# Performance work log

Hardware: AMD Instinct MI355X
Metric: run time of the kernel (lower is better)

## Reference

```python
import jax, jax.numpy as jnp
import numpy as np

NEG_SLOPE = 0.2  # LeakyReLU slope used by GAT attention
EPS = 1e-16


def gat_conv(x, edge_index, W, a_src, a_dst, b):
    """One GATConv layer with 'mean' head aggregation.
    x: [N, Fin], edge_index: [2, E] (row 0 = src/j, row 1 = dst/i),
    W: [Fin, H*F], a_src/a_dst: [H, F], b: [F].
    Returns [N, F].
    """
    N = x.shape[0]
    H, F = a_src.shape
    h = (x @ W).reshape(N, H, F)                      # [N, H, F]
    src, dst = edge_index[0], edge_index[1]
    # per-node attention halves, gathered per edge
    as_ = jnp.einsum('nhf,hf->nh', h, a_src)          # [N, H]
    ad_ = jnp.einsum('nhf,hf->nh', h, a_dst)          # [N, H]
    e = jax.nn.leaky_relu(as_[src] + ad_[dst], NEG_SLOPE)  # [E, H]
    # segment softmax over incoming edges of each dst node
    m = jax.ops.segment_max(e, dst, num_segments=N)   # [N, H]
    ex = jnp.exp(e - m[dst])                          # [E, H]
    denom = jax.ops.segment_sum(ex, dst, num_segments=N)
    alpha = ex / (denom[dst] + EPS)                   # [E, H]
    # weighted scatter-aggregate of source features
    out = jax.ops.segment_sum(alpha[:, :, None] * h[src], dst, num_segments=N)  # [N, H, F]
    return out.mean(axis=1) + b                       # mean over heads


def setup_inputs() -> dict:
    key = jax.random.key(0)
    ks = jax.random.split(key, 10)
    N, E = 100000, 1000000
    in_dim, hid, out_dim, H = 128, 32, 16, 4
    x = jax.random.normal(ks[0], (N, in_dim), dtype=jnp.float32)
    edge_index = jax.random.randint(ks[1], (2, E), 0, N, dtype=jnp.int64)
    s1 = 1.0 / np.sqrt(in_dim)
    s2 = 1.0 / np.sqrt(hid)
    W1 = jax.random.uniform(ks[2], (in_dim, H * hid), jnp.float32, -s1, s1)
    a1_src = jax.random.uniform(ks[3], (H, hid), jnp.float32, -s2, s2)
    a1_dst = jax.random.uniform(ks[4], (H, hid), jnp.float32, -s2, s2)
    b1 = jnp.zeros((hid,), jnp.float32)
    s3 = 1.0 / np.sqrt(out_dim)
    W2 = jax.random.uniform(ks[5], (hid, H * out_dim), jnp.float32, -s2, s2)
    a2_src = jax.random.uniform(ks[6], (H, out_dim), jnp.float32, -s3, s3)
    a2_dst = jax.random.uniform(ks[7], (H, out_dim), jnp.float32, -s3, s3)
    b2 = jnp.zeros((out_dim,), jnp.float32)
    return {"x": x, "edge_index": edge_index,
            "W1": W1, "a1_src": a1_src, "a1_dst": a1_dst, "b1": b1,
            "W2": W2, "a2_src": a2_src, "a2_dst": a2_dst, "b2": b2}


def reference(x, edge_index, W1, a1_src, a1_dst, b1, W2, a2_src, a2_dst, b2):
    h = gat_conv(x, edge_index, W1, a1_src, a1_dst, b1)
    h = jax.nn.relu(h)
    # dropout is identity in eval mode
    out = gat_conv(h, edge_index, W2, a2_src, a2_dst, b2)
    return out
```

## Files before the change

### kernel.cpp

```cpp
#include <hip/hip_runtime.h>
#include <math.h>

#define NEG_SLOPE 0.2f
#define EPS_GAT 1e-16f
#define LOG2E 1.4426950408889634f
typedef unsigned int u32;
typedef unsigned short u16;
typedef __attribute__((ext_vector_type(8))) short short8;
typedef __attribute__((ext_vector_type(4))) float f32x4;

__device__ inline u16 f2bf(float x) {
    union { float f; u32 u; } v; v.f = x;
    u32 r = v.u + 0x7FFFu + ((v.u >> 16) & 1u);
    return (u16)(r >> 16);
}
__device__ inline float bf_lo(u32 u) {
    union { u32 i; float f; } v; v.i = u << 16; return v.f;
}
__device__ inline float bf_hi(u32 u) {
    union { u32 i; float f; } v; v.i = u & 0xFFFF0000u; return v.f;
}
__device__ inline float bf1(u16 s) {
    union { u32 i; float f; } v; v.i = ((u32)s) << 16; return v.f;
}
__device__ inline float fast_exp2(float x) {
#if __has_builtin(__builtin_amdgcn_exp2f)
    return __builtin_amdgcn_exp2f(x);
#else
    return exp2f(x);
#endif
}
__device__ inline float lrelu_exp2(float t) {
    return fast_exp2(fmaxf(t, NEG_SLOPE * t));
}


__global__ void degree_kernel(const int* __restrict__ dst, int E,
                              int* __restrict__ counts, int* __restrict__ rank) {
    int e = blockIdx.x * blockDim.x + threadIdx.x;
    if (e < E) rank[e] = atomicAdd(&counts[dst[e]], 1);
}

__global__ __launch_bounds__(1024) void scan_block_kernel(const int* __restrict__ counts, int N,
                                                          int* __restrict__ scanned, int* __restrict__ bsums) {
    __shared__ int tmp[1024];
    int i = blockIdx.x * 1024 + threadIdx.x;
    int v = (i < N) ? counts[i] : 0;
    tmp[threadIdx.x] = v;
    __syncthreads();
    for (int d = 1; d < 1024; d <<= 1) {
        int t = (threadIdx.x >= d) ? tmp[threadIdx.x - d] : 0;
        __syncthreads();
        tmp[threadIdx.x] += t;
        __syncthreads();
    }
    if (i < N) scanned[i] = tmp[threadIdx.x];
    if (threadIdx.x == 1023) bsums[blockIdx.x] = tmp[1023];
}

__global__ __launch_bounds__(256) void scan_partials_kernel(int* __restrict__ bsums, int nb) {
    __shared__ int tmp[256];
    int tid = threadIdx.x;
    int v = (tid < nb) ? bsums[tid] : 0;
    tmp[tid] = v;
    __syncthreads();
    for (int d = 1; d < 256; d <<= 1) {
        int t = (tid >= d) ? tmp[tid - d] : 0;
        __syncthreads();
        tmp[tid] += t;
        __syncthreads();
    }
    if (tid < nb) bsums[tid] = tmp[tid] - v;
}

__global__ void finalize_offsets_kernel(const int* __restrict__ scanned,
                                        const int* __restrict__ bsums_excl, int N,
                                        int* __restrict__ row_off) {
    int i = blockIdx.x * blockDim.x + threadIdx.x;
    if (i < N) {
        int incl = scanned[i] + bsums_excl[i >> 10];
        row_off[i + 1] = incl;
        if (i == 0) row_off[0] = 0;
    }
}

__global__ void fill_csr_kernel(const int* __restrict__ src, const int* __restrict__ dst, int E,
                                const int* __restrict__ row_off, const int* __restrict__ rank,
                                int* __restrict__ csr_src) {
    int e = blockIdx.x * blockDim.x + threadIdx.x;
    if (e < E) {
        int pos = row_off[dst[e]] + rank[e];
        csr_src[pos] = src[e];
    }
}


__global__ void prep_kernel(const float* __restrict__ W1,
                            u16* __restrict__ w1t_hi, u16* __restrict__ w1t_lo,
                            const float* __restrict__ W2, const float* __restrict__ a2s,
                            const float* __restrict__ a2d, float* __restrict__ w_as,
                            float* __restrict__ w_ad) {
    if (blockIdx.x < 64) {
        int i = blockIdx.x * 256 + threadIdx.x;
        int k = i >> 7, n = i & 127;
        float w = W1[i];
        u16 hi = f2bf(w);
        u16 lo = f2bf(w - bf1(hi));
        w1t_hi[n * 128 + k] = hi;
        w1t_lo[n * 128 + k] = lo;
    } else {
        int t = threadIdx.x;
        if (t < 128) {
            int h = t >> 5, k = t & 31;
            float s1 = 0.f, s2 = 0.f;
#pragma unroll
            for (int f = 0; f < 16; ++f) {
                float w = W2[k * 64 + h * 16 + f];
                s1 += w * a2s[h * 16 + f];
                s2 += w * a2d[h * 16 + f];
            }
            w_as[h * 32 + k] = s1;
            w_ad[h * 32 + k] = s2;
        }
    }
}


__global__ __launch_bounds__(256) void gemm1_mfma_kernel(const float* __restrict__ X,
                                                         const u16* __restrict__ w1t_hi,
                                                         const u16* __restrict__ w1t_lo,
                                                         u16* __restrict__ Hb, int N) {
    __shared__ u16 xsh_hi[64][40];
    __shared__ u16 xsh_lo[64][40];
    __shared__ u16 wsh_hi[128][40];
    __shared__ u16 wsh_lo[128][40];
    int tid = threadIdx.x;
    int wave = tid >> 6, lane = tid & 63, quad = lane >> 4;
    int m0 = blockIdx.x * 64;

    f32x4 acc[4][2];
#pragma unroll
    for (int rt = 0; rt < 4; ++rt)
#pragma unroll
        for (int ct = 0; ct < 2; ++ct) acc[rt][ct] = (f32x4)(0.f);

    int xrow = tid >> 2, xkq = (tid & 3) * 8;

    for (int k0 = 0; k0 < 128; k0 += 32) {
        {
            int gr = m0 + xrow;
            float f[8];
            *(float4*)&f[0] = (gr < N) ? *(const float4*)(X + (size_t)gr * 128 + k0 + xkq)
                                       : make_float4(0.f, 0.f, 0.f, 0.f);
            *(float4*)&f[4] = (gr < N) ? *(const float4*)(X + (size_t)gr * 128 + k0 + xkq + 4)
                                       : make_float4(0.f, 0.f, 0.f, 0.f);
            u16 hi[8], lo[8];
#pragma unroll
            for (int i = 0; i < 8; ++i) {
                hi[i] = f2bf(f[i]);
                lo[i] = f2bf(f[i] - bf1(hi[i]));
            }
            *(uint4*)&xsh_hi[xrow][xkq] = *(uint4*)hi;
            *(uint4*)&xsh_lo[xrow][xkq] = *(uint4*)lo;
        }
        {
#pragma unroll
            for (int i = 0; i < 2; ++i) {
                int id = tid * 2 + i;
                int n = id >> 2, part = id & 3;
                *(uint4*)&wsh_hi[n][part * 8] =
                    ((const uint4*)(w1t_hi + n * 128 + k0))[part];
                *(uint4*)&wsh_lo[n][part * 8] =
                    ((const uint4*)(w1t_lo + n * 128 + k0))[part];
            }
        }
        __syncthreads();

        short8 bhi[2], blo[2];
#pragma unroll
        for (int ct = 0; ct < 2; ++ct) {
            int n = wave * 32 + ct * 16 + (lane & 15);
            bhi[ct] = *(const short8*)&wsh_hi[n][quad * 8];
            blo[ct] = *(const short8*)&wsh_lo[n][quad * 8];
        }
#pragma unroll
        for (int rt = 0; rt < 4; ++rt) {
            int m = rt * 16 + (lane & 15);
            short8 ahi = *(const short8*)&xsh_hi[m][quad * 8];
            short8 alo = *(const short8*)&xsh_lo[m][quad * 8];
#pragma unroll
            for (int ct = 0; ct < 2; ++ct) {
                acc[rt][ct] = __builtin_amdgcn_mfma_f32_16x16x32_bf16(ahi, bhi[ct], acc[rt][ct], 0, 0, 0);
                acc[rt][ct] = __builtin_amdgcn_mfma_f32_16x16x32_bf16(alo, bhi[ct], acc[rt][ct], 0, 0, 0);
                acc[rt][ct] = __builtin_amdgcn_mfma_f32_16x16x32_bf16(ahi, blo[ct], acc[rt][ct], 0, 0, 0);
            }
        }
        __syncthreads();
    }

#pragma unroll
    for (int rt = 0; rt < 4; ++rt)
#pragma unroll
        for (int ct = 0; ct < 2; ++ct) {
            int col = wave * 32 + ct * 16 + (lane & 15);
#pragma unroll
            for (int r = 0; r < 4; ++r) {
                int gr = m0 + rt * 16 + quad * 4 + r;
                if (gr < N) Hb[(size_t)gr * 128 + col] = f2bf(acc[rt][ct][r]);
            }
        }
}


__global__ void attn1_kernel(const u16* __restrict__ Hb, const float* __restrict__ a_src,
                             const float* __restrict__ a_dst, float* __restrict__ as_,
                             float* __restrict__ ad_, int N) {
    int t = blockIdx.x * blockDim.x + threadIdx.x;
    int n = t >> 2, h = t & 3;
    if (n >= N) return;
    const u32* hr = (const u32*)(Hb + (size_t)n * 128 + h * 32);
    const float* av = a_src + h * 32;
    const float* bv = a_dst + h * 32;
    float s1 = 0.f, s2 = 0.f;
#pragma unroll
    for (int q = 0; q < 4; ++q) {
        uint4 u = *(const uint4*)(hr + q * 4);
        float f0 = bf_lo(u.x), f1 = bf_hi(u.x);
        float f2 = bf_lo(u.y), f3 = bf_hi(u.y);
        float f4 = bf_lo(u.z), f5 = bf_hi(u.z);
        float f6 = bf_lo(u.w), f7 = bf_hi(u.w);
        int k = q * 8;
        s1 += f0 * av[k] + f1 * av[k + 1] + f2 * av[k + 2] + f3 * av[k + 3]
            + f4 * av[k + 4] + f5 * av[k + 5] + f6 * av[k + 6] + f7 * av[k + 7];
        s2 += f0 * bv[k] + f1 * bv[k + 1] + f2 * bv[k + 2] + f3 * bv[k + 3]
            + f4 * bv[k + 4] + f5 * bv[k + 5] + f6 * bv[k + 6] + f7 * bv[k + 7];
    }
    as_[n * 4 + h] = s1 * LOG2E;
    ad_[n * 4 + h] = s2 * LOG2E;
}


__global__ __launch_bounds__(256) void node_agg128_kernel(const u32* __restrict__ Hb,
                                                          const float* __restrict__ as_,
                                                          const float* __restrict__ ad_,
                                                          const int* __restrict__ row_off,
                                                          const int* __restrict__ csr_src,
                                                          const float* __restrict__ bias,
                                                          u32* __restrict__ O1, int N) {
    int lane = threadIdx.x & 63;
    int node = __builtin_amdgcn_readfirstlane(blockIdx.x * 4 + (threadIdx.x >> 6));
    if (node >= N) return;
    int start = __builtin_amdgcn_readfirstlane(row_off[node]);
    int end   = __builtin_amdgcn_readfirstlane(row_off[node + 1]);
    int deg = end - start;
    int h = lane >> 4;
    float adh = ad_[node * 4 + h];

    int clamp = (deg > 0) ? deg - 1 : 0;
    int vidx = csr_src[start + min(lane, clamp)];
    int m = min(deg, 64);

    float ax = 0.f, ay = 0.f, den = 0.f;
    int j = 0;
    for (; j + 4 <= m; j += 4) {
        int s0 = __builtin_amdgcn_readlane(vidx, j);
        int s1 = __builtin_amdgcn_readlane(vidx, j + 1);
        int s2 = __builtin_amdgcn_readlane(vidx, j + 2);
        int s3 = __builtin_amdgcn_readlane(vidx, j + 3);
        float a0 = as_[s0 * 4 + h], a1 = as_[s1 * 4 + h];
        float a2 = as_[s2 * 4 + h], a3 = as_[s3 * 4 + h];
        u32 u0 = Hb[s0 * 64 + lane];
        u32 u1 = Hb[s1 * 64 + lane];
        u32 u2 = Hb[s2 * 64 + lane];
        u32 u3 = Hb[s3 * 64 + lane];
        float e0 = lrelu_exp2(a0 + adh), e1 = lrelu_exp2(a1 + adh);
        float e2 = lrelu_exp2(a2 + adh), e3 = lrelu_exp2(a3 + adh);
        ax += e0 * bf_lo(u0); ay += e0 * bf_hi(u0); den += e0;
        ax += e1 * bf_lo(u1); ay += e1 * bf_hi(u1); den += e1;
        ax += e2 * bf_lo(u2); ay += e2 * bf_hi(u2); den += e2;
        ax += e3 * bf_lo(u3); ay += e3 * bf_hi(u3); den += e3;
    }
    for (; j < m; ++j) {
        int s = __builtin_amdgcn_readlane(vidx, j);
        float e = lrelu_exp2(as_[s * 4 + h] + adh);
        u32 u = Hb[s * 64 + lane];
        ax += e * bf_lo(u); ay += e * bf_hi(u); den += e;
    }
    for (int jj = start + 64; jj < end; ++jj) {
        int s = __builtin_amdgcn_readfirstlane(csr_src[jj]);
        float e = lrelu_exp2(as_[s * 4 + h] + adh);
        u32 u = Hb[s * 64 + lane];
        ax += e * bf_lo(u); ay += e * bf_hi(u); den += e;
    }
    float inv = 1.f / (den + EPS_GAT);
    float px = ax * inv, py = ay * inv;
    px += __shfl_xor(px, 16); py += __shfl_xor(py, 16);
    px += __shfl_xor(px, 32); py += __shfl_xor(py, 32);
    if (lane < 16) {
        int f = lane * 2;
        float ox = fmaxf(px * 0.25f + bias[f], 0.f);
        float oy = fmaxf(py * 0.25f + bias[f + 1], 0.f);
        O1[node * 16 + lane] = (u32)f2bf(ox) | ((u32)f2bf(oy) << 16);
    }
}


__global__ void attn2_kernel(const u32* __restrict__ O1, const float* __restrict__ w_as,
                             const float* __restrict__ w_ad, float* __restrict__ as_,
                             float* __restrict__ ad_, int N) {
    int t = blockIdx.x * blockDim.x + threadIdx.x;
    int n = t >> 2, h = t & 3;
    if (n >= N) return;
    const u32* r = O1 + (size_t)n * 16;
    const float* wa = w_as + h * 32;
    const float* wd = w_ad + h * 32;
    float s1 = 0.f, s2 = 0.f;
#pragma unroll
    for (int q = 0; q < 4; ++q) {
        uint4 u = *(const uint4*)(r + q * 4);
        float f0 = bf_lo(u.x), f1 = bf_hi(u.x);
        float f2 = bf_lo(u.y), f3 = bf_hi(u.y);
        float f4 = bf_lo(u.z), f5 = bf_hi(u.z);
        float f6 = bf_lo(u.w), f7 = bf_hi(u.w);
        int k = q * 8;
        s1 += f0 * wa[k] + f1 * wa[k + 1] + f2 * wa[k + 2] + f3 * wa[k + 3]
            + f4 * wa[k + 4] + f5 * wa[k + 5] + f6 * wa[k + 6] + f7 * wa[k + 7];
        s2 += f0 * wd[k] + f1 * wd[k + 1] + f2 * wd[k + 2] + f3 * wd[k + 3]
            + f4 * wd[k + 4] + f5 * wd[k + 5] + f6 * wd[k + 6] + f7 * wd[k + 7];
    }
    as_[n * 4 + h] = s1 * LOG2E;
    ad_[n * 4 + h] = s2 * LOG2E;
}


__global__ __launch_bounds__(256) void node_agg32_fused_kernel(const u32* __restrict__ O1,
                                                               const float* __restrict__ as_,
                                                               const float* __restrict__ ad_,
                                                               const int* __restrict__ row_off,
                                                               const int* __restrict__ csr_src,
                                                               const float* __restrict__ W2,
                                                               const float* __restrict__ b2,
                                                               float* __restrict__ Out, int N) {
    __shared__ float w2sh[2048];
    __shared__ float aggsh[4][136];
    int tid = threadIdx.x;
    {
        float4 v = ((const float4*)W2)[tid];
        *(float4*)&w2sh[tid * 4] = v;
        float4 v2 = ((const float4*)W2)[tid + 256];
        *(float4*)&w2sh[(tid + 256) * 4] = v2;
    }

    int lane = tid & 63;
    int nb = tid >> 6;
    int node = __builtin_amdgcn_readfirstlane(blockIdx.x * 4 + nb);
    bool active = node < N;
    int h = lane >> 4, f = lane & 15;
    if (active) {
        int start = __builtin_amdgcn_readfirstlane(row_off[node]);
        int end   = __builtin_amdgcn_readfirstlane(row_off[node + 1]);
        int deg = end - start;
        float adh = ad_[node * 4 + h];

        int clamp = (deg > 0) ? deg - 1 : 0;
        int vidx = csr_src[start + min(lane, clamp)];
        int m = min(deg, 64);

        float ax = 0.f, ay = 0.f, den = 0.f;
        int j = 0;
        for (; j + 4 <= m; j += 4) {
            int s0 = __builtin_amdgcn_readlane(vidx, j);
            int s1 = __builtin_amdgcn_readlane(vidx, j + 1);
            int s2 = __builtin_amdgcn_readlane(vidx, j + 2);
            int s3 = __builtin_amdgcn_readlane(vidx, j + 3);
            float a0 = as_[s0 * 4 + h], a1 = as_[s1 * 4 + h];
            float a2 = as_[s2 * 4 + h], a3 = as_[s3 * 4 + h];
            u32 u0 = O1[s0 * 16 + f];
            u32 u1 = O1[s1 * 16 + f];
            u32 u2 = O1[s2 * 16 + f];
            u32 u3 = O1[s3 * 16 + f];
            float e0 = lrelu_exp2(a0 + adh), e1 = lrelu_exp2(a1 + adh);
            float e2 = lrelu_exp2(a2 + adh), e3 = lrelu_exp2(a3 + adh);
            ax += e0 * bf_lo(u0); ay += e0 * bf_hi(u0); den += e0;
            ax += e1 * bf_lo(u1); ay += e1 * bf_hi(u1); den += e1;
            ax += e2 * bf_lo(u2); ay += e2 * bf_hi(u2); den += e2;
            ax += e3 * bf_lo(u3); ay += e3 * bf_hi(u3); den += e3;
        }
        for (; j < m; ++j) {
            int s = __builtin_amdgcn_readlane(vidx, j);
            float e = lrelu_exp2(as_[s * 4 + h] + adh);
            u32 u = O1[s * 16 + f];
            ax += e * bf_lo(u); ay += e * bf_hi(u); den += e;
        }
        for (int jj = start + 64; jj < end; ++jj) {
            int s = __builtin_amdgcn_readfirstlane(csr_src[jj]);
            float e = lrelu_exp2(as_[s * 4 + h] + adh);
            u32 u = O1[s * 16 + f];
            ax += e * bf_lo(u); ay += e * bf_hi(u); den += e;
        }
        float inv = 1.f / (den + EPS_GAT);
        aggsh[nb][h * 34 + f * 2]     = ax * inv;
        aggsh[nb][h * 34 + f * 2 + 1] = ay * inv;
    }
    __syncthreads();

    if (active) {
        int q = h, o = f;
        float s = 0.f;
#pragma unroll
        for (int k = 0; k < 32; ++k)
            s += aggsh[nb][q * 34 + k] * w2sh[k * 64 + q * 16 + o];
        s += __shfl_xor(s, 16);
        s += __shfl_xor(s, 32);
        if (lane < 16)
            Out[(size_t)node * 16 + o] = s * 0.25f + b2[o];
    }
}


extern "C" void kernel_launch(void* const* d_in, const int* in_sizes, int n_in,
                              void* d_out, int out_size, void* d_ws, size_t ws_size,
                              hipStream_t stream) {
    const float* x      = (const float*)d_in[0];
    const int*   eidx   = (const int*)d_in[1];
    const float* W1     = (const float*)d_in[2];
    const float* a1_src = (const float*)d_in[3];
    const float* a1_dst = (const float*)d_in[4];
    const float* b1     = (const float*)d_in[5];
    const float* W2     = (const float*)d_in[6];
    const float* a2_src = (const float*)d_in[7];
    const float* a2_dst = (const float*)d_in[8];
    const float* b2     = (const float*)d_in[9];
    float* out = (float*)d_out;

    const int N = in_sizes[0] / 128;
    const int E = in_sizes[1] / 2;
    const int* src = eidx;
    const int* dst = eidx + E;

    char* base = (char*)d_ws;
    size_t off = 0;
    auto carve = [&](size_t bytes) -> char* {
        off = (off + 255) & ~(size_t)255;
        char* p = base + off;
        off += bytes;
        return p;
    };
    int* counts   = (int*)carve((size_t)N * 4);
    int* scanned  = (int*)carve((size_t)N * 4);
    int* bsums    = (int*)carve(256 * 4);
    int* row_off  = (int*)carve((size_t)(N + 1) * 4);
    int* rank     = (int*)carve((size_t)E * 4);
    int* csr_src  = (int*)carve((size_t)E * 4);
    u16* w1t_hi   = (u16*)carve(128 * 128 * 2);
    u16* w1t_lo   = (u16*)carve(128 * 128 * 2);
    u16* h1b      = (u16*)carve((size_t)N * 128 * 2);
    u32* out1b    = (u32*)carve((size_t)N * 16 * 4);
    float* as1  = (float*)carve((size_t)N * 4 * 4);
    float* ad1  = (float*)carve((size_t)N * 4 * 4);
    float* as2  = (float*)carve((size_t)N * 4 * 4);
    float* ad2  = (float*)carve((size_t)N * 4 * 4);
    float* w_as = (float*)carve(4 * 32 * 4);
    float* w_ad = (float*)carve(4 * 32 * 4);
    (void)ws_size; (void)n_in; (void)out_size;

    hipMemsetAsync(counts, 0, (size_t)N * 4, stream);
    degree_kernel<<<(E + 255) / 256, 256, 0, stream>>>(dst, E, counts, rank);
    int nb = (N + 1023) / 1024;
    scan_block_kernel<<<nb, 1024, 0, stream>>>(counts, N, scanned, bsums);
    scan_partials_kernel<<<1, 256, 0, stream>>>(bsums, nb);
    finalize_offsets_kernel<<<(N + 255) / 256, 256, 0, stream>>>(scanned, bsums, N, row_off);
    fill_csr_kernel<<<(E + 255) / 256, 256, 0, stream>>>(src, dst, E, row_off, rank, csr_src);

    prep_kernel<<<65, 256, 0, stream>>>(W1, w1t_hi, w1t_lo, W2, a2_src, a2_dst, w_as, w_ad);

    gemm1_mfma_kernel<<<(N + 63) / 64, 256, 0, stream>>>(x, w1t_hi, w1t_lo, h1b, N);
    attn1_kernel<<<(N * 4 + 255) / 256, 256, 0, stream>>>(h1b, a1_src, a1_dst, as1, ad1, N);
    node_agg128_kernel<<<(N + 3) / 4, 256, 0, stream>>>((const u32*)h1b, as1, ad1,
                                                        row_off, csr_src, b1, out1b, N);

    attn2_kernel<<<(N * 4 + 255) / 256, 256, 0, stream>>>(out1b, w_as, w_ad, as2, ad2, N);
    node_agg32_fused_kernel<<<(N + 3) / 4, 256, 0, stream>>>(out1b, as2, ad2, row_off,
                                                             csr_src, W2, b2, out, N);
}
```

Baseline: 322.9 us.

## Fuse attention-score kernels into GEMM and layer-1 aggregation, merge prep with degree

```diff
diff --git a/kernel.cpp b/kernel.cpp
--- a/kernel.cpp
+++ b/kernel.cpp
@@ -35,73 +35,19 @@
 }
 
 
-__global__ void degree_kernel(const int* __restrict__ dst, int E,
-                              int* __restrict__ counts, int* __restrict__ rank) {
-    int e = blockIdx.x * blockDim.x + threadIdx.x;
-    if (e < E) rank[e] = atomicAdd(&counts[dst[e]], 1);
-}
-
-__global__ __launch_bounds__(1024) void scan_block_kernel(const int* __restrict__ counts, int N,
-                                                          int* __restrict__ scanned, int* __restrict__ bsums) {
-    __shared__ int tmp[1024];
-    int i = blockIdx.x * 1024 + threadIdx.x;
-    int v = (i < N) ? counts[i] : 0;
-    tmp[threadIdx.x] = v;
-    __syncthreads();
-    for (int d = 1; d < 1024; d <<= 1) {
-        int t = (threadIdx.x >= d) ? tmp[threadIdx.x - d] : 0;
-        __syncthreads();
-        tmp[threadIdx.x] += t;
-        __syncthreads();
-    }
-    if (i < N) scanned[i] = tmp[threadIdx.x];
-    if (threadIdx.x == 1023) bsums[blockIdx.x] = tmp[1023];
-}
-
-__global__ __launch_bounds__(256) void scan_partials_kernel(int* __restrict__ bsums, int nb) {
-    __shared__ int tmp[256];
-    int tid = threadIdx.x;
-    int v = (tid < nb) ? bsums[tid] : 0;
-    tmp[tid] = v;
-    __syncthreads();
-    for (int d = 1; d < 256; d <<= 1) {
-        int t = (tid >= d) ? tmp[tid - d] : 0;
-        __syncthreads();
-        tmp[tid] += t;
-        __syncthreads();
-    }
-    if (tid < nb) bsums[tid] = tmp[tid] - v;
-}
-
-__global__ void finalize_offsets_kernel(const int* __restrict__ scanned,
-                                        const int* __restrict__ bsums_excl, int N,
-                                        int* __restrict__ row_off) {
-    int i = blockIdx.x * blockDim.x + threadIdx.x;
-    if (i < N) {
-        int incl = scanned[i] + bsums_excl[i >> 10];
-        row_off[i + 1] = incl;
-        if (i == 0) row_off[0] = 0;
-    }
-}
-
-__global__ void fill_csr_kernel(const int* __restrict__ src, const int* __restrict__ dst, int E,
-                                const int* __restrict__ row_off, const int* __restrict__ rank,
-                                int* __restrict__ csr_src) {
-    int e = blockIdx.x * blockDim.x + threadIdx.x;
-    if (e < E) {
-        int pos = row_off[dst[e]] + rank[e];
-        csr_src[pos] = src[e];
-    }
-}
-
-
-__global__ void prep_kernel(const float* __restrict__ W1,
-                            u16* __restrict__ w1t_hi, u16* __restrict__ w1t_lo,
-                            const float* __restrict__ W2, const float* __restrict__ a2s,
-                            const float* __restrict__ a2d, float* __restrict__ w_as,
-                            float* __restrict__ w_ad) {
-    if (blockIdx.x < 64) {
-        int i = blockIdx.x * 256 + threadIdx.x;
+__global__ void degree_prep_kernel(const int* __restrict__ dst, int E,
+                                   int* __restrict__ counts, int* __restrict__ rank,
+                                   const float* __restrict__ W1,
+                                   u16* __restrict__ w1t_hi, u16* __restrict__ w1t_lo,
+                                   const float* __restrict__ W2, const float* __restrict__ a2s,
+                                   const float* __restrict__ a2d, float* __restrict__ w_as,
+                                   float* __restrict__ w_ad, int degBlocks) {
+    int b = blockIdx.x;
+    if (b < degBlocks) {
+        int e = b * 256 + threadIdx.x;
+        if (e < E) rank[e] = atomicAdd(&counts[dst[e]], 1);
+    } else if (b < degBlocks + 64) {
+        int i = (b - degBlocks) * 256 + threadIdx.x;
         int k = i >> 7, n = i & 127;
         float w = W1[i];
         u16 hi = f2bf(w);
@@ -125,18 +71,79 @@
     }
 }
 
+__global__ __launch_bounds__(1024) void scan_block_kernel(const int* __restrict__ counts, int N,
+                                                          int* __restrict__ scanned, int* __restrict__ bsums) {
+    __shared__ int tmp[1024];
+    int i = blockIdx.x * 1024 + threadIdx.x;
+    int v = (i < N) ? counts[i] : 0;
+    tmp[threadIdx.x] = v;
+    __syncthreads();
+    for (int d = 1; d < 1024; d <<= 1) {
+        int t = (threadIdx.x >= d) ? tmp[threadIdx.x - d] : 0;
+        __syncthreads();
+        tmp[threadIdx.x] += t;
+        __syncthreads();
+    }
+    if (i < N) scanned[i] = tmp[threadIdx.x];
+    if (threadIdx.x == 1023) bsums[blockIdx.x] = tmp[1023];
+}
+
+__global__ __launch_bounds__(256) void scan_partials_kernel(int* __restrict__ bsums, int nb) {
+    __shared__ int tmp[256];
+    int tid = threadIdx.x;
+    int v = (tid < nb) ? bsums[tid] : 0;
+    tmp[tid] = v;
+    __syncthreads();
+    for (int d = 1; d < 256; d <<= 1) {
+        int t = (tid >= d) ? tmp[tid - d] : 0;
+        __syncthreads();
+        tmp[tid] += t;
+        __syncthreads();
+    }
+    if (tid < nb) bsums[tid] = tmp[tid] - v;
+}
+
+__global__ void finalize_offsets_kernel(const int* __restrict__ scanned,
+                                        const int* __restrict__ bsums_excl, int N,
+                                        int* __restrict__ row_off) {
+    int i = blockIdx.x * blockDim.x + threadIdx.x;
+    if (i < N) {
+        int incl = scanned[i] + bsums_excl[i >> 10];
+        row_off[i + 1] = incl;
+        if (i == 0) row_off[0] = 0;
+    }
+}
+
+__global__ void fill_csr_kernel(const int* __restrict__ src, const int* __restrict__ dst, int E,
+                                const int* __restrict__ row_off, const int* __restrict__ rank,
+                                int* __restrict__ csr_src) {
+    int e = blockIdx.x * blockDim.x + threadIdx.x;
+    if (e < E) {
+        int pos = row_off[dst[e]] + rank[e];
+        csr_src[pos] = src[e];
+    }
+}
+
 
 __global__ __launch_bounds__(256) void gemm1_mfma_kernel(const float* __restrict__ X,
                                                          const u16* __restrict__ w1t_hi,
                                                          const u16* __restrict__ w1t_lo,
-                                                         u16* __restrict__ Hb, int N) {
+                                                         const float* __restrict__ a_src,
+                                                         const float* __restrict__ a_dst,
+                                                         u16* __restrict__ Hb,
+                                                         float* __restrict__ as_,
+                                                         float* __restrict__ ad_, int N) {
     __shared__ u16 xsh_hi[64][40];
     __shared__ u16 xsh_lo[64][40];
-    __shared__ u16 wsh_hi[128][40];
-    __shared__ u16 wsh_lo[128][40];
+    __shared__ u16 wbuf[10240];
+    __shared__ float ash[128], adsh[128];
+    u16* wsh_hi = wbuf;
+    u16* wsh_lo = wbuf + 5120;
     int tid = threadIdx.x;
     int wave = tid >> 6, lane = tid & 63, quad = lane >> 4;
     int m0 = blockIdx.x * 64;
+
+    if (tid < 128) { ash[tid] = a_src[tid]; adsh[tid] = a_dst[tid]; }
 
     f32x4 acc[4][2];
 #pragma unroll
@@ -168,9 +175,9 @@
             for (int i = 0; i < 2; ++i) {
                 int id = tid * 2 + i;
                 int n = id >> 2, part = id & 3;
-                *(uint4*)&wsh_hi[n][part * 8] =
+                *(uint4*)&wsh_hi[n * 40 + part * 8] =
                     ((const uint4*)(w1t_hi + n * 128 + k0))[part];
-                *(uint4*)&wsh_lo[n][part * 8] =
+                *(uint4*)&wsh_lo[n * 40 + part * 8] =
                     ((const uint4*)(w1t_lo + n * 128 + k0))[part];
             }
         }
@@ -180,8 +187,8 @@
 #pragma unroll
         for (int ct = 0; ct < 2; ++ct) {
             int n = wave * 32 + ct * 16 + (lane & 15);
-            bhi[ct] = *(const short8*)&wsh_hi[n][quad * 8];
-            blo[ct] = *(const short8*)&wsh_lo[n][quad * 8];
+            bhi[ct] = *(const short8*)&wsh_hi[n * 40 + quad * 8];
+            blo[ct] = *(const short8*)&wsh_lo[n * 40 + quad * 8];
         }
 #pragma unroll
         for (int rt = 0; rt < 4; ++rt) {
@@ -198,6 +205,7 @@
         __syncthreads();
     }
 
+    const int HS = 130;
 #pragma unroll
     for (int rt = 0; rt < 4; ++rt)
 #pragma unroll
@@ -205,38 +213,32 @@
             int col = wave * 32 + ct * 16 + (lane & 15);
 #pragma unroll
             for (int r = 0; r < 4; ++r) {
-                int gr = m0 + rt * 16 + quad * 4 + r;
-                if (gr < N) Hb[(size_t)gr * 128 + col] = f2bf(acc[rt][ct][r]);
-            }
-        }
-}
-
-
-__global__ void attn1_kernel(const u16* __restrict__ Hb, const float* __restrict__ a_src,
-                             const float* __restrict__ a_dst, float* __restrict__ as_,
-                             float* __restrict__ ad_, int N) {
-    int t = blockIdx.x * blockDim.x + threadIdx.x;
-    int n = t >> 2, h = t & 3;
-    if (n >= N) return;
-    const u32* hr = (const u32*)(Hb + (size_t)n * 128 + h * 32);
-    const float* av = a_src + h * 32;
-    const float* bv = a_dst + h * 32;
-    float s1 = 0.f, s2 = 0.f;
-#pragma unroll
-    for (int q = 0; q < 4; ++q) {
-        uint4 u = *(const uint4*)(hr + q * 4);
-        float f0 = bf_lo(u.x), f1 = bf_hi(u.x);
-        float f2 = bf_lo(u.y), f3 = bf_hi(u.y);
-        float f4 = bf_lo(u.z), f5 = bf_hi(u.z);
-        float f6 = bf_lo(u.w), f7 = bf_hi(u.w);
-        int k = q * 8;
-        s1 += f0 * av[k] + f1 * av[k + 1] + f2 * av[k + 2] + f3 * av[k + 3]
-            + f4 * av[k + 4] + f5 * av[k + 5] + f6 * av[k + 6] + f7 * av[k + 7];
-        s2 += f0 * bv[k] + f1 * bv[k + 1] + f2 * bv[k + 2] + f3 * bv[k + 3]
-            + f4 * bv[k + 4] + f5 * bv[k + 5] + f6 * bv[k + 6] + f7 * bv[k + 7];
-    }
-    as_[n * 4 + h] = s1 * LOG2E;
-    ad_[n * 4 + h] = s2 * LOG2E;
+                int row = rt * 16 + quad * 4 + r;
+                u16 hv = f2bf(acc[rt][ct][r]);
+                int gr = m0 + row;
+                if (gr < N) Hb[(size_t)gr * 128 + col] = hv;
+                wbuf[row * HS + col] = hv;
+            }
+        }
+    __syncthreads();
+
+    {
+        int row = tid >> 2, h = tid & 3;
+        int gr = m0 + row;
+        if (gr < N) {
+            const u32* hr = (const u32*)&wbuf[row * HS + h * 32];
+            float s1 = 0.f, s2 = 0.f;
+#pragma unroll
+            for (int q = 0; q < 16; ++q) {
+                u32 u = hr[q];
+                float flo = bf_lo(u), fhi = bf_hi(u);
+                s1 += flo * ash[h * 32 + 2 * q] + fhi * ash[h * 32 + 2 * q + 1];
+                s2 += flo * adsh[h * 32 + 2 * q] + fhi * adsh[h * 32 + 2 * q + 1];
+            }
+            as_[(size_t)gr * 4 + h] = s1 * LOG2E;
+            ad_[(size_t)gr * 4 + h] = s2 * LOG2E;
+        }
+    }
 }
 
 
@@ -246,7 +248,11 @@
                                                           const int* __restrict__ row_off,
                                                           const int* __restrict__ csr_src,
                                                           const float* __restrict__ bias,
-                                                          u32* __restrict__ O1, int N) {
+                                                          const float* __restrict__ w_as,
+                                                          const float* __restrict__ w_ad,
+                                                          u32* __restrict__ O1,
+                                                          float* __restrict__ as2,
+                                                          float* __restrict__ ad2, int N) {
     int lane = threadIdx.x & 63;
     int node = __builtin_amdgcn_readfirstlane(blockIdx.x * 4 + (threadIdx.x >> 6));
     if (node >= N) return;
@@ -260,7 +266,8 @@
     int vidx = csr_src[start + min(lane, clamp)];
     int m = min(deg, 64);
 
-    float ax = 0.f, ay = 0.f, den = 0.f;
+    float2 acc = make_float2(0.f, 0.f);
+    float den = 0.f;
     int j = 0;
     for (; j + 4 <= m; j += 4) {
         int s0 = __builtin_amdgcn_readlane(vidx, j);
@@ -275,61 +282,48 @@
         u32 u3 = Hb[s3 * 64 + lane];
         float e0 = lrelu_exp2(a0 + adh), e1 = lrelu_exp2(a1 + adh);
         float e2 = lrelu_exp2(a2 + adh), e3 = lrelu_exp2(a3 + adh);
-        ax += e0 * bf_lo(u0); ay += e0 * bf_hi(u0); den += e0;
-        ax += e1 * bf_lo(u1); ay += e1 * bf_hi(u1); den += e1;
-        ax += e2 * bf_lo(u2); ay += e2 * bf_hi(u2); den += e2;
-        ax += e3 * bf_lo(u3); ay += e3 * bf_hi(u3); den += e3;
+        acc.x = fmaf(e0, bf_lo(u0), acc.x); acc.y = fmaf(e0, bf_hi(u0), acc.y); den += e0;
+        acc.x = fmaf(e1, bf_lo(u1), acc.x); acc.y = fmaf(e1, bf_hi(u1), acc.y); den += e1;
+        acc.x = fmaf(e2, bf_lo(u2), acc.x); acc.y = fmaf(e2, bf_hi(u2), acc.y); den += e2;
+        acc.x = fmaf(e3, bf_lo(u3), acc.x); acc.y = fmaf(e3, bf_hi(u3), acc.y); den += e3;
     }
     for (; j < m; ++j) {
         int s = __builtin_amdgcn_readlane(vidx, j);
         float e = lrelu_exp2(as_[s * 4 + h] + adh);
         u32 u = Hb[s * 64 + lane];
-        ax += e * bf_lo(u); ay += e * bf_hi(u); den += e;
+        acc.x = fmaf(e, bf_lo(u), acc.x); acc.y = fmaf(e, bf_hi(u), acc.y); den += e;
     }
     for (int jj = start + 64; jj < end; ++jj) {
         int s = __builtin_amdgcn_readfirstlane(csr_src[jj]);
         float e = lrelu_exp2(as_[s * 4 + h] + adh);
         u32 u = Hb[s * 64 + lane];
-        ax += e * bf_lo(u); ay += e * bf_hi(u); den += e;
+        acc.x = fmaf(e, bf_lo(u), acc.x); acc.y = fmaf(e, bf_hi(u), acc.y); den += e;
     }
     float inv = 1.f / (den + EPS_GAT);
-    float px = ax * inv, py = ay * inv;
+    float px = acc.x * inv, py = acc.y * inv;
     px += __shfl_xor(px, 16); py += __shfl_xor(py, 16);
     px += __shfl_xor(px, 32); py += __shfl_xor(py, 32);
-    if (lane < 16) {
-        int f = lane * 2;
-        float ox = fmaxf(px * 0.25f + bias[f], 0.f);
-        float oy = fmaxf(py * 0.25f + bias[f + 1], 0.f);
+
+    int f2 = (lane & 15) * 2;
+    float2 bv = *(const float2*)&bias[f2];
+    float ox = fmaxf(px * 0.25f + bv.x, 0.f);
+    float oy = fmaxf(py * 0.25f + bv.y, 0.f);
+    if (lane < 16)
         O1[node * 16 + lane] = (u32)f2bf(ox) | ((u32)f2bf(oy) << 16);
-    }
-}
-
-
-__global__ void attn2_kernel(const u32* __restrict__ O1, const float* __restrict__ w_as,
-                             const float* __restrict__ w_ad, float* __restrict__ as_,
-                             float* __restrict__ ad_, int N) {
-    int t = blockIdx.x * blockDim.x + threadIdx.x;
-    int n = t >> 2, h = t & 3;
-    if (n >= N) return;
-    const u32* r = O1 + (size_t)n * 16;
-    const float* wa = w_as + h * 32;
-    const float* wd = w_ad + h * 32;
-    float s1 = 0.f, s2 = 0.f;
-#pragma unroll
-    for (int q = 0; q < 4; ++q) {
-        uint4 u = *(const uint4*)(r + q * 4);
-        float f0 = bf_lo(u.x), f1 = bf_hi(u.x);
-        float f2 = bf_lo(u.y), f3 = bf_hi(u.y);
-        float f4 = bf_lo(u.z), f5 = bf_hi(u.z);
-        float f6 = bf_lo(u.w), f7 = bf_hi(u.w);
-        int k = q * 8;
-        s1 += f0 * wa[k] + f1 * wa[k + 1] + f2 * wa[k + 2] + f3 * wa[k + 3]
-            + f4 * wa[k + 4] + f5 * wa[k + 5] + f6 * wa[k + 6] + f7 * wa[k + 7];
-        s2 += f0 * wd[k] + f1 * wd[k + 1] + f2 * wd[k + 2] + f3 * wd[k + 3]
-            + f4 * wd[k + 4] + f5 * wd[k + 5] + f6 * wd[k + 6] + f7 * wd[k + 7];
-    }
-    as_[n * 4 + h] = s1 * LOG2E;
-    ad_[n * 4 + h] = s2 * LOG2E;
+
+    int h2 = lane >> 4;
+    float2 wa = *(const float2*)&w_as[h2 * 32 + f2];
+    float2 wd = *(const float2*)&w_ad[h2 * 32 + f2];
+    float ta = ox * wa.x + oy * wa.y;
+    float td = ox * wd.x + oy * wd.y;
+    ta += __shfl_xor(ta, 1); td += __shfl_xor(td, 1);
+    ta += __shfl_xor(ta, 2); td += __shfl_xor(td, 2);
+    ta += __shfl_xor(ta, 4); td += __shfl_xor(td, 4);
+    ta += __shfl_xor(ta, 8); td += __shfl_xor(td, 8);
+    if ((lane & 15) == 0) {
+        as2[node * 4 + h2] = ta * LOG2E;
+        ad2[node * 4 + h2] = td * LOG2E;
+    }
 }
 
 
@@ -366,7 +360,8 @@
         int vidx = csr_src[start + min(lane, clamp)];
         int m = min(deg, 64);
 
-        float ax = 0.f, ay = 0.f, den = 0.f;
+        float2 acc = make_float2(0.f, 0.f);
+        float den = 0.f;
         int j = 0;
         for (; j + 4 <= m; j += 4) {
             int s0 = __builtin_amdgcn_readlane(vidx, j);
@@ -381,26 +376,26 @@
             u32 u3 = O1[s3 * 16 + f];
             float e0 = lrelu_exp2(a0 + adh), e1 = lrelu_exp2(a1 + adh);
             float e2 = lrelu_exp2(a2 + adh), e3 = lrelu_exp2(a3 + adh);
-            ax += e0 * bf_lo(u0); ay += e0 * bf_hi(u0); den += e0;
-            ax += e1 * bf_lo(u1); ay += e1 * bf_hi(u1); den += e1;
-            ax += e2 * bf_lo(u2); ay += e2 * bf_hi(u2); den += e2;
-            ax += e3 * bf_lo(u3); ay += e3 * bf_hi(u3); den += e3;
+            acc.x = fmaf(e0, bf_lo(u0), acc.x); acc.y = fmaf(e0, bf_hi(u0), acc.y); den += e0;
+            acc.x = fmaf(e1, bf_lo(u1), acc.x); acc.y = fmaf(e1, bf_hi(u1), acc.y); den += e1;
+            acc.x = fmaf(e2, bf_lo(u2), acc.x); acc.y = fmaf(e2, bf_hi(u2), acc.y); den += e2;
+            acc.x = fmaf(e3, bf_lo(u3), acc.x); acc.y = fmaf(e3, bf_hi(u3), acc.y); den += e3;
         }
         for (; j < m; ++j) {
             int s = __builtin_amdgcn_readlane(vidx, j);
             float e = lrelu_exp2(as_[s * 4 + h] + adh);
             u32 u = O1[s * 16 + f];
-            ax += e * bf_lo(u); ay += e * bf_hi(u); den += e;
+            acc.x = fmaf(e, bf_lo(u), acc.x); acc.y = fmaf(e, bf_hi(u), acc.y); den += e;
         }
         for (int jj = start + 64; jj < end; ++jj) {
             int s = __builtin_amdgcn_readfirstlane(csr_src[jj]);
             float e = lrelu_exp2(as_[s * 4 + h] + adh);
             u32 u = O1[s * 16 + f];
-            ax += e * bf_lo(u); ay += e * bf_hi(u); den += e;
+            acc.x = fmaf(e, bf_lo(u), acc.x); acc.y = fmaf(e, bf_hi(u), acc.y); den += e;
         }
         float inv = 1.f / (den + EPS_GAT);
-        aggsh[nb][h * 34 + f * 2]     = ax * inv;
-        aggsh[nb][h * 34 + f * 2 + 1] = ay * inv;
+        aggsh[nb][h * 34 + f * 2]     = acc.x * inv;
+        aggsh[nb][h * 34 + f * 2 + 1] = acc.y * inv;
     }
     __syncthreads();
 
@@ -465,21 +460,23 @@
     (void)ws_size; (void)n_in; (void)out_size;
 
     hipMemsetAsync(counts, 0, (size_t)N * 4, stream);
-    degree_kernel<<<(E + 255) / 256, 256, 0, stream>>>(dst, E, counts, rank);
+    int degBlocks = (E + 255) / 256;
+    degree_prep_kernel<<<degBlocks + 65, 256, 0, stream>>>(dst, E, counts, rank,
+                                                           W1, w1t_hi, w1t_lo,
+                                                           W2, a2_src, a2_dst, w_as, w_ad,
+                                                           degBlocks);
     int nb = (N + 1023) / 1024;
     scan_block_kernel<<<nb, 1024, 0, stream>>>(counts, N, scanned, bsums);
     scan_partials_kernel<<<1, 256, 0, stream>>>(bsums, nb);
     finalize_offsets_kernel<<<(N + 255) / 256, 256, 0, stream>>>(scanned, bsums, N, row_off);
     fill_csr_kernel<<<(E + 255) / 256, 256, 0, stream>>>(src, dst, E, row_off, rank, csr_src);
 
-    prep_kernel<<<65, 256, 0, stream>>>(W1, w1t_hi, w1t_lo, W2, a2_src, a2_dst, w_as, w_ad);
-
-    gemm1_mfma_kernel<<<(N + 63) / 64, 256, 0, stream>>>(x, w1t_hi, w1t_lo, h1b, N);
-    attn1_kernel<<<(N * 4 + 255) / 256, 256, 0, stream>>>(h1b, a1_src, a1_dst, as1, ad1, N);
+    gemm1_mfma_kernel<<<(N + 63) / 64, 256, 0, stream>>>(x, w1t_hi, w1t_lo, a1_src, a1_dst,
+                                                         h1b, as1, ad1, N);
     node_agg128_kernel<<<(N + 3) / 4, 256, 0, stream>>>((const u32*)h1b, as1, ad1,
-                                                        row_off, csr_src, b1, out1b, N);
-
-    attn2_kernel<<<(N * 4 + 255) / 256, 256, 0, stream>>>(out1b, w_as, w_ad, as2, ad2, N);
+                                                        row_off, csr_src, b1, w_as, w_ad,
+                                                        out1b, as2, ad2, N);
+
     node_agg32_fused_kernel<<<(N + 3) / 4, 256, 0, stream>>>(out1b, as2, ad2, row_off,
                                                              csr_src, W2, b2, out, N);
 }
```

New measurement: 298.5 us (median of 2 runs). 7.6% less time.
